# Optimization experiments

Hardware: AMD Instinct MI355X
Metric: run time of the kernel (lower is better)

The kernel has to match this reference:

```python
import jax, jax.numpy as jnp
import numpy as np

# FPN level layout for a 1024x1024 input image
LEVEL_HW = [(128, 128), (64, 64), (32, 32), (16, 16), (8, 8)]
STRIDES = [8, 16, 32, 64, 128]
IMG = 1024.0
NUM_CLASSES = 80
SCORE_THRESH = 0.2
NMS_THRESH = 0.6
TOPK = 1000
DETS = 100
BATCH = 8
TOTAL = sum(h * w for h, w in LEVEL_HW)  # 21824


def _make_anchors():
    rows = []
    for (h, w), s in zip(LEVEL_HW, STRIDES):
        xs = (np.arange(w, dtype=np.float32) + 0.5) * s
        ys = (np.arange(h, dtype=np.float32) + 0.5) * s
        xx, yy = np.meshgrid(xs, ys, indexing='ij')  # x-major, matches transpose(2,3) flatten
        pts = np.stack([xx.ravel(), yy.ravel(), xx.ravel(), yy.ravel()], axis=1)
        rows.append(pts)
    return np.concatenate(rows, axis=0).astype(np.float32)


def setup_inputs() -> dict:
    key = jax.random.key(0)
    k1, k2, k3 = jax.random.split(key, 3)
    cls_logits = jax.random.normal(k1, (BATCH, TOTAL, NUM_CLASSES), dtype=jnp.float32)
    bbox_regression = jax.random.uniform(k2, (BATCH, TOTAL, 4), dtype=jnp.float32) * 64.0
    bbox_ctrness = jax.random.normal(k3, (BATCH, TOTAL, 1), dtype=jnp.float32)
    anchors = jnp.asarray(_make_anchors())
    return {"cls_logits": cls_logits, "bbox_regression": bbox_regression,
            "bbox_ctrness": bbox_ctrness, "anchors": anchors}


def _iou_matrix(b):
    # b: [N,4] -> [N,N] pairwise IoU
    area = jnp.clip(b[:, 2] - b[:, 0], 0) * jnp.clip(b[:, 3] - b[:, 1], 0)
    lt = jnp.maximum(b[:, None, :2], b[None, :, :2])
    rb = jnp.minimum(b[:, None, 2:], b[None, :, 2:])
    wh = jnp.clip(rb - lt, 0)
    inter = wh[..., 0] * wh[..., 1]
    union = area[:, None] + area[None, :] - inter
    return inter / jnp.maximum(union, 1e-9)


def _postprocess_one(logits, reg, ctr, anchors):
    boxes_l, scores_l, labels_l = [], [], []
    off = 0
    for (h, w) in LEVEL_HW:
        n = h * w
        lg = logits[off:off + n]          # [n, C]
        rg = reg[off:off + n]             # [n, 4]
        ct = ctr[off:off + n, 0]          # [n]
        an = anchors[off:off + n]         # [n, 4]
        vals = lg.max(axis=-1)
        cls = jnp.argmax(lg, axis=-1)
        sc = jnp.sqrt(jax.nn.sigmoid(vals) * jax.nn.sigmoid(ct))
        # masked threshold + top-k  ==  filter-then-topk of the original
        masked = jnp.where(sc > SCORE_THRESH, sc, -1.0)
        k = min(TOPK, n)
        tv, ti = jax.lax.top_k(masked, k)
        a = an[ti]
        r = rg[ti]
        cx = (a[:, 0] + a[:, 2]) * 0.5
        cy = (a[:, 1] + a[:, 3]) * 0.5
        bx = jnp.stack([cx - r[:, 0], cy - r[:, 1], cx + r[:, 2], cy + r[:, 3]], axis=-1)
        bx = jnp.clip(bx, 0.0, IMG)       # clip_boxes_to_image
        boxes_l.append(bx)
        scores_l.append(tv)
        labels_l.append(cls[ti])
        off += n
    boxes = jnp.concatenate(boxes_l, axis=0)    # [N,4], N=3320
    scores = jnp.concatenate(scores_l, axis=0)  # [N]
    labels = jnp.concatenate(labels_l, axis=0)  # [N]
    N = boxes.shape[0]
    valid = scores > SCORE_THRESH
    order = jnp.argsort(-scores)
    boxes = boxes[order]
    scores = scores[order]
    labels = labels[order]
    valid = valid[order]
    # batched_nms: offset boxes per class so cross-class IoU is 0
    boff = boxes + (labels.astype(boxes.dtype) * (IMG + 1.0))[:, None]
    iou = _iou_matrix(boff)
    idx = jnp.arange(N)
    def body(i, active):
        sup = (iou[i] > NMS_THRESH) & (idx > i) & active[i]
        return active & ~sup
    active = jax.lax.fori_loop(0, N, body, valid)
    fsc = jnp.where(active, scores, -jnp.inf)
    tv, ti = jax.lax.top_k(fsc, DETS)
    m = tv > SCORE_THRESH
    out_boxes = jnp.where(m[:, None], boxes[ti], 0.0)
    out_scores = jnp.where(m, tv, 0.0)
    out_labels = jnp.where(m, labels[ti], -1)
    return out_boxes, out_scores, out_labels


def reference(cls_logits, bbox_regression, bbox_ctrness, anchors):
    fn = lambda l, r, c: _postprocess_one(l, r, c, anchors)
    boxes, scores, labels = jax.vmap(fn)(cls_logits, bbox_regression, bbox_ctrness)
    return boxes, scores, labels
```

## Files before the change

### kernel.cpp

```cpp
#include <hip/hip_runtime.h>
#include <stdint.h>

typedef unsigned long long u64;
typedef unsigned int u32;

#define BATCH   8
#define TOTAL   21824
#define NCLS    80
#define NDET    100
#define IMGSZ   1024.0f
#define STHR    0.2f
#define NMST    0.6f
#define NBUCK   4096
#define BMAX    4031
#define KGLOB   1000
#define NLOC    22
#define PRE     1024
#define ZN      ((BATCH * NBUCK) / 4)

__device__ __forceinline__ float sigm(float x) { return 1.0f / (1.0f + expf(-x)); }

__device__ __forceinline__ u32 mapKm(float s) {
    u32 u = __float_as_uint(s);
    u32 m = u ^ ((u & 0x80000000u) ? 0xFFFFFFFFu : 0x80000000u);
    return ~m;
}
__device__ __forceinline__ float unmapKm(u32 km) {
    return __uint_as_float((~km) ^ 0x80000000u);
}
__device__ __forceinline__ u64 makeKey(float s, u32 idx) {
    return (((u64)mapKm(s)) << 32) | (u64)idx;
}

__device__ __forceinline__ int bucketOfV(float s) {
    int b = (int)(__fmul_rn(__fsub_rn(1.0f, s), 5040.0f));
    return b > BMAX ? BMAX : b;
}

__device__ __forceinline__ bool suppress(float4 a, float4 c) {
    float aa = __fmul_rn(fmaxf(__fsub_rn(a.z, a.x), 0.f), fmaxf(__fsub_rn(a.w, a.y), 0.f));
    float ac = __fmul_rn(fmaxf(__fsub_rn(c.z, c.x), 0.f), fmaxf(__fsub_rn(c.w, c.y), 0.f));
    float ltx = fmaxf(a.x, c.x), lty = fmaxf(a.y, c.y);
    float rbx = fminf(a.z, c.z), rby = fminf(a.w, c.w);
    float iw = fmaxf(__fsub_rn(rbx, ltx), 0.f), ih = fmaxf(__fsub_rn(rby, lty), 0.f);
    float inter = __fmul_rn(iw, ih);
    float uni = __fsub_rn(__fadd_rn(aa, ac), inter);
    float iou = __fdiv_rn(inter, fmaxf(uni, 1e-9f));
    return iou > NMST;
}

__global__ __launch_bounds__(256) void zero_hist(u32* __restrict__ g) {
    int i = blockIdx.x * 256 + threadIdx.x;
    if (i < ZN) ((uint4*)g)[i] = make_uint4(0u, 0u, 0u, 0u);
}

__global__ __launch_bounds__(256) void score_kernel(
        const float* __restrict__ logits, const float* __restrict__ ctr,
        float* __restrict__ mscore, u32* __restrict__ ghist) {
    const int b = blockIdx.y;
    const int tid = threadIdx.x;
    const int wave = tid >> 6, lane = tid & 63;
    const int g = lane >> 2, j = lane & 3;
    const int rowBase = blockIdx.x * 256 + wave * 64;

    int r[4]; bool valid[4];
#pragma unroll
    for (int t = 0; t < 4; t++) {
        int rr = rowBase + 16 * t + g;
        valid[t] = rr < TOTAL;
        r[t] = valid[t] ? rr : (TOTAL - 1);
    }
    float4 vv[20]; float cc[4];
#pragma unroll
    for (int t = 0; t < 4; t++) {
        const float* rowp = logits + ((size_t)b * TOTAL + r[t]) * NCLS + j * 4;
#pragma unroll
        for (int u = 0; u < 5; u++)
            vv[t * 5 + u] = *(const float4*)(rowp + u * 16);
    }
#pragma unroll
    for (int t = 0; t < 4; t++) cc[t] = ctr[(size_t)b * TOTAL + r[t]];

#pragma unroll
    for (int t = 0; t < 4; t++) {
        float m0 = -1e30f;
#pragma unroll
        for (int u = 0; u < 5; u++) {
            float4 v = vv[t * 5 + u];
            m0 = fmaxf(m0, fmaxf(fmaxf(v.x, v.y), fmaxf(v.z, v.w)));
        }
        m0 = fmaxf(m0, __shfl_xor(m0, 1));
        m0 = fmaxf(m0, __shfl_xor(m0, 2));
        if (valid[t] && j == 0) {
            float sc = sqrtf(sigm(m0) * sigm(cc[t]));
            bool pass = sc > STHR;
            mscore[(size_t)b * TOTAL + r[t]] = pass ? sc : -1.0f;
            if (pass) atomicAdd(&ghist[(size_t)b * NBUCK + bucketOfV(sc)], 1u);
        }
    }
}

__device__ __forceinline__ int rowLabel(const float4* __restrict__ row4) {
    float best = -1e30f;
#pragma unroll
    for (int k = 0; k < 20; k++) {
        float4 q = row4[k];
        best = fmaxf(best, fmaxf(fmaxf(q.x, q.y), fmaxf(q.z, q.w)));
    }
    int lb = -1;
#pragma unroll
    for (int k = 0; k < 20; k++) {
        float4 q = row4[k];
        if (lb < 0) {
            if      (q.x == best) lb = 4 * k;
            else if (q.y == best) lb = 4 * k + 1;
            else if (q.z == best) lb = 4 * k + 2;
            else if (q.w == best) lb = 4 * k + 3;
        }
    }
    return lb;
}

__global__ __launch_bounds__(1024) void nms_kernel(
        const float* __restrict__ mscore, const float* __restrict__ logits,
        const float* __restrict__ anchors, const float* __restrict__ reg,
        const u32* __restrict__ ghist, float* __restrict__ out) {
    __shared__ u64 skey[2048];
    __shared__ float4 preB[PRE];
    __shared__ u32 curbuf[NBUCK];
    __shared__ int preL[PRE];
    __shared__ u32 waveSum[16], waveOff[16];
    __shared__ u32 sh_B, sh_m;
    __shared__ int s_count;
    __shared__ float4 accB[NDET];
    __shared__ float4 accR[NDET];
    __shared__ float  accS[NDET];
    __shared__ int    accL[NDET];
    __shared__ float4 wb[64], wraw[64];
    __shared__ int    wLab[64];
    __shared__ u64 wsup[64];
    __shared__ u64 sRej[16];

    const int b = blockIdx.x, tid = threadIdx.x;
    const int wave = tid >> 6, lane = tid & 63;
    const float* ms = mscore + (size_t)b * TOTAL;
    const float4* anch4 = (const float4*)anchors;
    const float4* reg4 = ((const float4*)reg) + (size_t)b * TOTAL;
    const float* lg = logits + (size_t)b * TOTAL * NCLS;

    uint4 hv = ((const uint4*)(ghist + (size_t)b * NBUCK))[tid];

    float sv[NLOC];
#pragma unroll
    for (int k = 0; k < NLOC; k++) {
        int i = tid + (k << 10);
        sv[k] = (i < TOTAL) ? ms[i] : -1.0f;
    }

    u32 h0 = hv.x, h1 = hv.y, h2 = hv.z, h3 = hv.w;
    u32 s = h0 + h1 + h2 + h3;
    u32 incl = s;
    for (int o = 1; o < 64; o <<= 1) {
        u32 t2 = (u32)__shfl_up((int)incl, o);
        if (lane >= o) incl += t2;
    }
    if (lane == 63) waveSum[wave] = incl;
    __syncthreads();
    if (tid == 0) {
        u32 acc = 0;
#pragma unroll
        for (int w = 0; w < 16; w++) { waveOff[w] = acc; acc += waveSum[w]; }
        sh_m = acc;
        sh_B = (u32)BMAX;
        s_count = 0;
    }
    __syncthreads();
    {
        const u32 E = waveOff[wave] + incl - s;
        const u32 p1 = E + h0, p2 = p1 + h1, p3 = p2 + h2, p4 = p3 + h3;
        if      (E  < KGLOB && KGLOB <= p1) { sh_B = (u32)(4 * tid);     sh_m = p1; }
        else if (p1 < KGLOB && KGLOB <= p2) { sh_B = (u32)(4 * tid + 1); sh_m = p2; }
        else if (p2 < KGLOB && KGLOB <= p3) { sh_B = (u32)(4 * tid + 2); sh_m = p3; }
        else if (p3 < KGLOB && KGLOB <= p4) { sh_B = (u32)(4 * tid + 3); sh_m = p4; }
    }
    curbuf[tid] = 0; curbuf[tid + 1024] = 0; curbuf[tid + 2048] = 0; curbuf[tid + 3072] = 0;
    __syncthreads();
    const int Bstar = (int)sh_B;

    const float sLo = 1.0f - (float)(Bstar + 2) * (1.0f / 5040.0f);
    const u32 kmMin = mapKm(1.0f);
    const u32 kmMax = mapKm(sLo);
    const u32 range = kmMax - kmMin + 1u;
    int hib = 32 - __clz(range);
    const int fsh = hib > 12 ? hib - 12 : 0;

#pragma unroll
    for (int k = 0; k < NLOC; k++) {
        float s0 = sv[k];
        if (s0 > STHR && bucketOfV(s0) <= Bstar) {
            u32 fb = (mapKm(s0) - kmMin) >> fsh;
            if (fb > 4095u) fb = 4095u;
            atomicAdd(&curbuf[fb], 1u);
        }
    }
    __syncthreads();

    u32 f0 = curbuf[4 * tid], f1 = curbuf[4 * tid + 1],
        f2 = curbuf[4 * tid + 2], f3 = curbuf[4 * tid + 3];
    u32 fs = f0 + f1 + f2 + f3;
    u32 fincl = fs;
    for (int o = 1; o < 64; o <<= 1) {
        u32 t2 = (u32)__shfl_up((int)fincl, o);
        if (lane >= o) fincl += t2;
    }
    __syncthreads();
    if (lane == 63) waveSum[wave] = fincl;
    __syncthreads();
    if (tid == 0) {
        u32 acc = 0;
#pragma unroll
        for (int w = 0; w < 16; w++) { waveOff[w] = acc; acc += waveSum[w]; }
    }
    __syncthreads();
    const u32 E2 = waveOff[wave] + fincl - fs;
    const u32 q1 = E2 + f0, q2 = q1 + f1, q3 = q2 + f2;
    curbuf[4 * tid]     = E2;
    curbuf[4 * tid + 1] = q1;
    curbuf[4 * tid + 2] = q2;
    curbuf[4 * tid + 3] = q3;
    __syncthreads();

#pragma unroll
    for (int k = 0; k < NLOC; k++) {
        float s0 = sv[k];
        if (s0 > STHR && bucketOfV(s0) <= Bstar) {
            u32 fb = (mapKm(s0) - kmMin) >> fsh;
            if (fb > 4095u) fb = 4095u;
            int pos = (int)atomicAdd(&curbuf[fb], 1u);
            if (pos < 2048) skey[pos] = makeKey(s0, (u32)(tid + (k << 10)));
        }
    }
    __syncthreads();
    float4* preR = (float4*)curbuf;

#pragma unroll
    for (int q = 0; q < 4; q++) {
        u32 cnt = (q == 0) ? f0 : (q == 1) ? f1 : (q == 2) ? f2 : f3;
        u32 lo0 = (q == 0) ? E2 : (q == 1) ? q1 : (q == 2) ? q2 : q3;
        if (cnt > 1) {
            int lo = (int)lo0;
            int hi = lo + (int)cnt; if (hi > 2048) hi = 2048;
            for (int i2 = lo + 1; i2 < hi; i2++) {
                u64 key = skey[i2];
                int j2 = i2 - 1;
                while (j2 >= lo && skey[j2] > key) { skey[j2 + 1] = skey[j2]; j2--; }
                skey[j2 + 1] = key;
            }
        }
    }
    __syncthreads();
    int m = (int)sh_m; if (m > 2048) m = 2048;
    const int Pm = m < PRE ? m : PRE;

    for (int p = tid; p < Pm; p += 1024) {
        u64 key = skey[p];
        int idx = (int)(key & 0xFFFFFFFFu);
        float4 a = anch4[idx];
        float4 r = reg4[idx];
        int lb = rowLabel((const float4*)(lg + (size_t)idx * NCLS));
        float cx = (a.x + a.z) * 0.5f;
        float cy = (a.y + a.w) * 0.5f;
        float x1 = fminf(fmaxf(cx - r.x, 0.0f), IMGSZ);
        float y1 = fminf(fmaxf(cy - r.y, 0.0f), IMGSZ);
        float x2 = fminf(fmaxf(cx + r.z, 0.0f), IMGSZ);
        float y2 = fminf(fmaxf(cy + r.w, 0.0f), IMGSZ);
        float off = (float)lb * (IMGSZ + 1.0f);
        preR[p] = make_float4(x1, y1, x2, y2);
        preB[p] = make_float4(__fadd_rn(x1, off), __fadd_rn(y1, off),
                              __fadd_rn(x2, off), __fadd_rn(y2, off));
        preL[p] = lb;
    }
    __syncthreads();

    int count = 0, Ew = 0;
    while (true) {
        int take = m - Ew; if (take > 64) take = 64;
        if (take <= 0) break;
        const bool ldsPath = (Ew + take <= Pm);

        if (!ldsPath) {
            if (tid < take) {
                int idx = (int)(skey[Ew + tid] & 0xFFFFFFFFu);
                float4 a = anch4[idx];
                float4 r = reg4[idx];
                int lb = rowLabel((const float4*)(lg + (size_t)idx * NCLS));
                float cx = (a.x + a.z) * 0.5f;
                float cy = (a.y + a.w) * 0.5f;
                float x1 = fminf(fmaxf(cx - r.x, 0.0f), IMGSZ);
                float y1 = fminf(fmaxf(cy - r.y, 0.0f), IMGSZ);
                float x2 = fminf(fmaxf(cx + r.z, 0.0f), IMGSZ);
                float y2 = fminf(fmaxf(cy + r.w, 0.0f), IMGSZ);
                float off = (float)lb * (IMGSZ + 1.0f);
                wraw[tid] = make_float4(x1, y1, x2, y2);
                wb[tid] = make_float4(__fadd_rn(x1, off), __fadd_rn(y1, off),
                                      __fadd_rn(x2, off), __fadd_rn(y2, off));
                wLab[tid] = lb;
            }
            __syncthreads();
        }

        {
            float4 myB;
            if (lane < take) myB = ldsPath ? preB[Ew + lane] : wb[lane];
            bool rej = false;
            if (lane < take) {
                for (int s2 = wave; s2 < count; s2 += 16) {
                    if (suppress(accB[s2], myB)) { rej = true; break; }
                }
            }
            u64 mask = __ballot(rej);
            if (lane == 0) sRej[wave] = mask;
            for (int rr = wave; rr < take; rr += 16) {
                float4 rB = ldsPath ? preB[Ew + rr] : wb[rr];
                bool sp = (lane < take && lane > rr) ? suppress(rB, myB) : false;
                u64 msk = __ballot(sp);
                if (lane == 0) wsup[rr] = msk;
            }
        }
        __syncthreads();

        if (wave == 0) {
            u64 rj = (lane < 16) ? sRej[lane] : 0ull;
#pragma unroll
            for (int o = 1; o < 64; o <<= 1) rj |= __shfl_xor(rj, o);
            u64 supr = (lane < take) ? wsup[lane] : 0ull;
            u64 validb = (take >= 64) ? ~0ull : ((1ull << take) - 1ull);
            u64 aliveM = validb & ~rj;
            u64 contrib = ((aliveM >> lane) & 1ull) ? supr : 0ull;
            u64 U = contrib;
#pragma unroll
            for (int o = 1; o < 64; o <<= 1) U |= __shfl_xor(U, o);
            int space = NDET - count;
            u64 accM;
            if ((U & aliveM) == 0ull) {
                accM = aliveM;
            } else {
                u64 rem = aliveM; accM = 0ull;
                while (rem) {
                    int rr = __builtin_ctzll(rem);
                    accM |= 1ull << rr;
                    if (__popcll(accM) >= space) break;
                    u64 sr = __shfl(supr, rr);
                    rem &= ~(1ull << rr);
                    rem &= ~sr;
                }
            }
            int na = __popcll(accM);
            int takeA = na < space ? na : space;
            if (lane < take && ((accM >> lane) & 1ull)) {
                int pos = __popcll(accM & ((1ull << lane) - 1ull));
                if (pos < takeA) {
                    int o2 = count + pos;
                    u64 key = skey[Ew + lane];
                    accB[o2] = ldsPath ? preB[Ew + lane] : wb[lane];
                    accR[o2] = ldsPath ? preR[Ew + lane] : wraw[lane];
                    accL[o2] = ldsPath ? preL[Ew + lane] : wLab[lane];
                    accS[o2] = unmapKm((u32)(key >> 32));
                }
            }
            if (lane == 0) s_count = count + takeA;
        }
        __syncthreads();
        count = s_count;
        Ew += take;
        if (count >= NDET) break;
    }
    __syncthreads();

    for (int s2 = tid; s2 < NDET; s2 += 1024) {
        float4 bxv = make_float4(0.f, 0.f, 0.f, 0.f);
        float scv = 0.0f, lbv = -1.0f;
        if (s2 < count) {
            bxv = accR[s2];
            scv = accS[s2];
            lbv = (float)accL[s2];
        }
        ((float4*)out)[b * NDET + s2] = bxv;
        out[BATCH * NDET * 4 + b * NDET + s2] = scv;
        out[BATCH * NDET * 4 + BATCH * NDET + b * NDET + s2] = lbv;
    }
}

extern "C" void kernel_launch(void* const* d_in, const int* in_sizes, int n_in,
                              void* d_out, int out_size, void* d_ws, size_t ws_size,
                              hipStream_t stream) {
    (void)in_sizes; (void)n_in; (void)out_size; (void)ws_size;
    const float* logits  = (const float*)d_in[0];
    const float* reg     = (const float*)d_in[1];
    const float* ctr     = (const float*)d_in[2];
    const float* anchors = (const float*)d_in[3];
    float* out = (float*)d_out;

    char* ws = (char*)d_ws;
    size_t off = 0;
    auto alloc = [&](size_t bytes) -> void* {
        off = (off + 255) & ~(size_t)255;
        void* p = ws + off;
        off += bytes;
        return p;
    };
    float* mscore = (float*)alloc((size_t)BATCH * TOTAL * 4);
    u32*   ghist  = (u32*)  alloc((size_t)BATCH * NBUCK * 4);

    zero_hist<<<dim3((ZN + 255) / 256), 256, 0, stream>>>(ghist);
    score_kernel<<<dim3((TOTAL + 255) / 256, BATCH), 256, 0, stream>>>(logits, ctr, mscore, ghist);
    nms_kernel<<<BATCH, 1024, 0, stream>>>(mscore, logits, anchors, reg, ghist, out);
}
```

Measured before the change: 127.0 us.

## Scatter passing score keys into per-segment global buckets during scoring

The score kernel no longer writes a dense masked score array. Each passing anchor now appends its packed (score, index) key into one of 64 coarse score segments, using a global atomic counter per segment. The NMS kernel then reads only the segments up to the one holding the top-1000 cutoff, instead of every thread loading 22 scores and filtering them. This trades a full per-batch score scan inside the single-block NMS kernel for extra returning global atomics and scattered 8-byte writes in the score kernel, plus a much larger workspace.

```diff
diff --git a/kernel.cpp b/kernel.cpp
--- a/kernel.cpp
+++ b/kernel.cpp
@@ -14,9 +14,10 @@
 #define NBUCK   4096
 #define BMAX    4031
 #define KGLOB   1000
-#define NLOC    22
+#define NSEG    64
+#define CSTRIDE 16
 #define PRE     1024
-#define ZN      ((BATCH * NBUCK) / 4)
+#define ZN      ((BATCH * NBUCK + BATCH * NSEG * CSTRIDE) / 4)
 
 __device__ __forceinline__ float sigm(float x) { return 1.0f / (1.0f + expf(-x)); }
 
@@ -56,7 +57,7 @@
 
 __global__ __launch_bounds__(256) void score_kernel(
         const float* __restrict__ logits, const float* __restrict__ ctr,
-        float* __restrict__ mscore, u32* __restrict__ ghist) {
+        u32* __restrict__ ghist, u32* __restrict__ gcur, u64* __restrict__ gseg) {
     const int b = blockIdx.y;
     const int tid = threadIdx.x;
     const int wave = tid >> 6, lane = tid & 63;
@@ -93,9 +94,14 @@
         m0 = fmaxf(m0, __shfl_xor(m0, 2));
         if (valid[t] && j == 0) {
             float sc = sqrtf(sigm(m0) * sigm(cc[t]));
-            bool pass = sc > STHR;
-            mscore[(size_t)b * TOTAL + r[t]] = pass ? sc : -1.0f;
-            if (pass) atomicAdd(&ghist[(size_t)b * NBUCK + bucketOfV(sc)], 1u);
+            if (sc > STHR) {
+                int bk = bucketOfV(sc);
+                atomicAdd(&ghist[(size_t)b * NBUCK + bk], 1u);
+                int seg = bk >> 6;
+                u32 pos = atomicAdd(&gcur[((size_t)b * NSEG + seg) * CSTRIDE], 1u);
+                if (pos < (u32)TOTAL)
+                    gseg[((size_t)b * NSEG + seg) * TOTAL + pos] = makeKey(sc, (u32)r[t]);
+            }
         }
     }
 }
@@ -122,13 +128,15 @@
 }
 
 __global__ __launch_bounds__(1024) void nms_kernel(
-        const float* __restrict__ mscore, const float* __restrict__ logits,
-        const float* __restrict__ anchors, const float* __restrict__ reg,
-        const u32* __restrict__ ghist, float* __restrict__ out) {
+        const float* __restrict__ logits, const float* __restrict__ anchors,
+        const float* __restrict__ reg, const u32* __restrict__ ghist,
+        const u32* __restrict__ gcur, const u64* __restrict__ gseg,
+        float* __restrict__ out) {
     __shared__ u64 skey[2048];
     __shared__ float4 preB[PRE];
     __shared__ u32 curbuf[NBUCK];
     __shared__ int preL[PRE];
+    __shared__ u32 segc[NSEG];
     __shared__ u32 waveSum[16], waveOff[16];
     __shared__ u32 sh_B, sh_m;
     __shared__ int s_count;
@@ -143,19 +151,12 @@
 
     const int b = blockIdx.x, tid = threadIdx.x;
     const int wave = tid >> 6, lane = tid & 63;
-    const float* ms = mscore + (size_t)b * TOTAL;
     const float4* anch4 = (const float4*)anchors;
     const float4* reg4 = ((const float4*)reg) + (size_t)b * TOTAL;
     const float* lg = logits + (size_t)b * TOTAL * NCLS;
 
     uint4 hv = ((const uint4*)(ghist + (size_t)b * NBUCK))[tid];
-
-    float sv[NLOC];
-#pragma unroll
-    for (int k = 0; k < NLOC; k++) {
-        int i = tid + (k << 10);
-        sv[k] = (i < TOTAL) ? ms[i] : -1.0f;
-    }
+    if (tid < NSEG) segc[tid] = gcur[((size_t)b * NSEG + tid) * CSTRIDE];
 
     u32 h0 = hv.x, h1 = hv.y, h2 = hv.z, h3 = hv.w;
     u32 s = h0 + h1 + h2 + h3;
@@ -186,6 +187,7 @@
     curbuf[tid] = 0; curbuf[tid + 1024] = 0; curbuf[tid + 2048] = 0; curbuf[tid + 3072] = 0;
     __syncthreads();
     const int Bstar = (int)sh_B;
+    const int Sstar = Bstar >> 6;
 
     const float sLo = 1.0f - (float)(Bstar + 2) * (1.0f / 5040.0f);
     const u32 kmMin = mapKm(1.0f);
@@ -194,13 +196,16 @@
     int hib = 32 - __clz(range);
     const int fsh = hib > 12 ? hib - 12 : 0;
 
-#pragma unroll
-    for (int k = 0; k < NLOC; k++) {
-        float s0 = sv[k];
-        if (s0 > STHR && bucketOfV(s0) <= Bstar) {
-            u32 fb = (mapKm(s0) - kmMin) >> fsh;
-            if (fb > 4095u) fb = 4095u;
-            atomicAdd(&curbuf[fb], 1u);
+    for (int sgi = 0; sgi <= Sstar; sgi++) {
+        int c = (int)segc[sgi];
+        const u64* sp = gseg + ((size_t)b * NSEG + sgi) * TOTAL;
+        for (int i = tid; i < c; i += 1024) {
+            u32 km = (u32)(sp[i] >> 32);
+            if (bucketOfV(unmapKm(km)) <= Bstar) {
+                u32 fb = (km - kmMin) >> fsh;
+                if (fb > 4095u) fb = 4095u;
+                atomicAdd(&curbuf[fb], 1u);
+            }
         }
     }
     __syncthreads();
@@ -230,14 +235,18 @@
     curbuf[4 * tid + 3] = q3;
     __syncthreads();
 
-#pragma unroll
-    for (int k = 0; k < NLOC; k++) {
-        float s0 = sv[k];
-        if (s0 > STHR && bucketOfV(s0) <= Bstar) {
-            u32 fb = (mapKm(s0) - kmMin) >> fsh;
-            if (fb > 4095u) fb = 4095u;
-            int pos = (int)atomicAdd(&curbuf[fb], 1u);
-            if (pos < 2048) skey[pos] = makeKey(s0, (u32)(tid + (k << 10)));
+    for (int sgi = 0; sgi <= Sstar; sgi++) {
+        int c = (int)segc[sgi];
+        const u64* sp = gseg + ((size_t)b * NSEG + sgi) * TOTAL;
+        for (int i = tid; i < c; i += 1024) {
+            u64 key = sp[i];
+            u32 km = (u32)(key >> 32);
+            if (bucketOfV(unmapKm(km)) <= Bstar) {
+                u32 fb = (km - kmMin) >> fsh;
+                if (fb > 4095u) fb = 4095u;
+                int pos = (int)atomicAdd(&curbuf[fb], 1u);
+                if (pos < 2048) skey[pos] = key;
+            }
         }
     }
     __syncthreads();
@@ -409,10 +418,11 @@
         off += bytes;
         return p;
     };
-    float* mscore = (float*)alloc((size_t)BATCH * TOTAL * 4);
-    u32*   ghist  = (u32*)  alloc((size_t)BATCH * NBUCK * 4);
+    u32* ghist = (u32*)alloc((size_t)BATCH * NBUCK * 4);
+    u32* gcur  = (u32*)alloc((size_t)BATCH * NSEG * CSTRIDE * 4);
+    u64* gseg  = (u64*)alloc((size_t)BATCH * NSEG * TOTAL * 8);
 
     zero_hist<<<dim3((ZN + 255) / 256), 256, 0, stream>>>(ghist);
-    score_kernel<<<dim3((TOTAL + 255) / 256, BATCH), 256, 0, stream>>>(logits, ctr, mscore, ghist);
-    nms_kernel<<<BATCH, 1024, 0, stream>>>(mscore, logits, anchors, reg, ghist, out);
-}
+    score_kernel<<<dim3((TOTAL + 255) / 256, BATCH), 256, 0, stream>>>(logits, ctr, ghist, gcur, gseg);
+    nms_kernel<<<BATCH, 1024, 0, stream>>>(logits, anchors, reg, ghist, gcur, gseg, out);
+}
```

Result: slower. 148.5 us (+16.9%).
